# Performance work log

Measured on AMD Instinct MI355X. Metric: run time of the kernel, lower is better.

Reference implementation:

```python
import jax, jax.numpy as jnp
import numpy as np

B, V, M, H = 256, 128, 256, 1024
TIMING_DIM = 10          # ceil(log2(max_timesteps=1024))
DECAY_ALPHA = 0.99
IN_DIM = (V + TIMING_DIM + 1 + 1) * M  # 35840


def setup_inputs() -> dict:
    key = jax.random.key(0)
    ks = jax.random.split(key, 12)
    x = jax.random.uniform(ks[0], (B, V), dtype=jnp.float32)
    memory = jax.random.uniform(ks[1], (B, M, V), dtype=jnp.float32)
    memory_timings = jax.random.randint(ks[2], (B, M), 0, 1000).astype(jnp.int64)
    memory_surprise = jax.random.uniform(ks[3], (B, M), dtype=jnp.float32)
    last_prediction = jax.random.uniform(ks[4], (B, V), dtype=jnp.float32)
    s1 = 1.0 / np.sqrt(IN_DIM)
    s2 = 1.0 / np.sqrt(H)
    W1 = jax.random.uniform(ks[5], (IN_DIM, H), dtype=jnp.float32, minval=-s1, maxval=s1)
    b1 = jnp.zeros((H,), jnp.float32)
    Wg = jax.random.uniform(ks[6], (IN_DIM, H), dtype=jnp.float32, minval=-s1, maxval=s1)
    bg = jnp.zeros((H,), jnp.float32)
    W2 = jax.random.uniform(ks[7], (H, V), dtype=jnp.float32, minval=-s2, maxval=s2)
    b2 = jnp.zeros((V,), jnp.float32)
    return {"x": x, "memory": memory, "memory_timings": memory_timings,
            "memory_surprise": memory_surprise, "last_prediction": last_prediction,
            "W1": W1, "b1": b1, "Wg": Wg, "bg": bg, "W2": W2, "b2": b2}


def _step(x, memory, memory_timings, memory_surprise, last_prediction):
    # surprise of incoming token under last prediction
    surprise = -jnp.log(jnp.sum(x * last_prediction, axis=1) + 1e-8)  # [B]
    # age + decay
    timings = memory_timings + 1
    surp = memory_surprise * DECAY_ALPHA
    # ring-buffer roll, write newest at slot 0
    mem = jnp.roll(memory, 1, axis=1).at[:, 0, :].set(x)
    timings = jnp.roll(timings, 1, axis=1).at[:, 0].set(0)
    surp = jnp.roll(surp, 1, axis=1).at[:, 0].set(surprise)
    # sort by age ascending, gather memory/surprise
    idx = jnp.argsort(timings, axis=1)                               # [B,M]
    sorted_timings = jnp.take_along_axis(timings, idx, axis=1)       # [B,M]
    sorted_memory = jnp.take_along_axis(mem, idx[..., None], axis=1)  # [B,M,V]
    sorted_surprise = jnp.take_along_axis(surp, idx, axis=1)          # [B,M]
    # binary encode timings
    powers = 2 ** jnp.arange(TIMING_DIM, dtype=sorted_timings.dtype)
    bits = ((sorted_timings[..., None] // powers) % 2).astype(jnp.float32)  # [B,M,T]
    norm_t = sorted_timings.astype(jnp.float32) / (
        jnp.max(sorted_timings, axis=1, keepdims=True).astype(jnp.float32) + 1.0)
    pred_input = jnp.concatenate(
        [sorted_memory.reshape(B, -1), bits.reshape(B, -1),
         norm_t.reshape(B, -1), sorted_surprise.reshape(B, -1)], axis=1)  # [B, IN_DIM]
    return pred_input


def reference(x, memory, memory_timings, memory_surprise, last_prediction,
              W1, b1, Wg, bg, W2, b2):
    pred_input = _step(x, memory, memory_timings, memory_surprise, last_prediction)
    # gated dense network: h = (xW1+b1) * sigmoid(xWg+bg); logits = hW2+b2
    h = (pred_input @ W1 + b1) * jax.nn.sigmoid(pred_input @ Wg + bg)
    return h @ W2 + b2
```

## Files before the change

### kernel.cpp

```cpp
#include <hip/hip_runtime.h>
#include <stdint.h>
#include <math.h>

#define BB 256
#define VV 128
#define MM 256
#define TDIM 10
#define HH 1024
#define IN_DIM 35840
#define KSPLIT 16
#define KSLICE 2240
#define BK 64
#define NCHUNK 35

using f32x4  = __attribute__((ext_vector_type(4))) float;
using bf16x8 = __attribute__((ext_vector_type(8))) short;

__device__ __forceinline__ unsigned short f2bf(float f) {
    unsigned int u = __float_as_uint(f);
    unsigned int r = (u + 0x7FFFu + ((u >> 16) & 1u)) >> 16;
    return (unsigned short)r;
}

__device__ __forceinline__ void gload_lds16(const void* g, void* l) {
    __builtin_amdgcn_global_load_lds(
        (const __attribute__((address_space(1))) unsigned int*)g,
        (__attribute__((address_space(3))) unsigned int*)l,
        16, 0, 0);
}

__global__ __launch_bounds__(256)
void k_build(const float* __restrict__ x, const float* __restrict__ memory,
             const int* __restrict__ timings, const float* __restrict__ msurp,
             const float* __restrict__ lastp, short* __restrict__ A)
{
    int b = blockIdx.x, t = threadIdx.x;
    __shared__ int t_s[MM], idx_s[MM], st_s[MM];
    __shared__ float red[MM];
    __shared__ float s_surprise;

    t_s[t] = (t == 0) ? 0 : timings[b*MM + t - 1] + 1;
    red[t] = (t < VV) ? x[b*VV + t] * lastp[b*VV + t] : 0.f;
    __syncthreads();
    for (int s = 128; s > 0; s >>= 1) {
        if (t < s) red[t] += red[t + s];
        __syncthreads();
    }
    if (t == 0) s_surprise = -logf(red[0] + 1e-8f);

    int ti = t_s[t], cnt = 0;
    #pragma unroll 4
    for (int j = 0; j < MM; ++j) {
        int tj = t_s[j];
        cnt += (tj < ti) || (tj == ti && j < t);
    }
    idx_s[cnt] = t;
    st_s[cnt]  = ti;
    __syncthreads();

    float invm = 1.f / ((float)st_s[MM-1] + 1.f);
    short* Ab = A + (size_t)b * IN_DIM;
    {
        int st = st_s[t], src = idx_s[t];
        #pragma unroll
        for (int tt = 0; tt < TDIM; ++tt)
            Ab[32768 + t*TDIM + tt] = (short)f2bf((float)((st >> tt) & 1));
        Ab[35328 + t] = (short)f2bf((float)st * invm);
        float sv = (src == 0) ? s_surprise : msurp[b*MM + src - 1] * 0.99f;
        Ab[35584 + t] = (short)f2bf(sv);
    }
    int half = t >> 7, v = t & (VV-1);
    for (int p = half; p < MM; p += 2) {
        int src = idx_s[p];
        float val = (src == 0) ? x[b*VV + v]
                               : memory[((size_t)b*MM + src - 1)*VV + v];
        Ab[p*VV + v] = (short)f2bf(val);
    }
}

__global__ __launch_bounds__(256, 4)
void k_gemm(const short* __restrict__ A, const float* __restrict__ W1,
            const float* __restrict__ Wg, float* __restrict__ P)
{
    int ks = blockIdx.x;
    int xt = blockIdx.y;
    const float* W = (xt < 32) ? W1 : Wg;
    int wcol0 = (xt & 31) * 32;
    int pcol0 = xt * 32;
    int k0 = ks * KSLICE;

    __shared__ bf16x8 As8[2048];
    __shared__ bf16x8 Ws8[256];

    int t = threadIdx.x;
    int l = t & 63, wv = t >> 6;
    int r = l & 15, q = l >> 4;

    int aoff[4][2], boff[2][2];
    #pragma unroll
    for (int mt = 0; mt < 4; ++mt)
        #pragma unroll
        for (int s = 0; s < 2; ++s)
            aoff[mt][s] = (wv*64 + mt*16 + r)*8 + ((q + 4*s) ^ (r & 7));
    #pragma unroll
    for (int nt = 0; nt < 2; ++nt)
        #pragma unroll
        for (int s = 0; s < 2; ++s)
            boff[nt][s] = (nt*16 + r)*8 + ((q + 4*s) ^ (r & 7));

    f32x4 acc[4][2];
    #pragma unroll
    for (int mt = 0; mt < 4; ++mt)
        #pragma unroll
        for (int nt = 0; nt < 2; ++nt)
            acc[mt][nt] = (f32x4){0.f, 0.f, 0.f, 0.f};

    int wn = t & 31, wkg = t >> 5;
    const float* wbase = W + (size_t)(k0 + wkg*8)*HH + wcol0 + wn;

    float wreg[8];
    #pragma unroll
    for (int j = 0; j < 8; ++j) wreg[j] = wbase[(size_t)j*HH];

    for (int c = 0; c < NCHUNK; ++c) {
        int kc = k0 + c*BK;
        __syncthreads();
        {
            union { bf16x8 v; unsigned int d[4]; } u;
            #pragma unroll
            for (int j = 0; j < 4; ++j)
                u.d[j] = (unsigned int)f2bf(wreg[2*j]) |
                         ((unsigned int)f2bf(wreg[2*j+1]) << 16);
            Ws8[wn*8 + (wkg ^ (wn & 7))] = u.v;
        }
        #pragma unroll
        for (int i = 0; i < 8; ++i) {
            int G = t + i*256;
            int m = G >> 3;
            int kb = (G & 7) ^ (m & 7);
            const short* gp = A + (size_t)m*IN_DIM + kc + kb*8;
            gload_lds16(gp, (void*)(As8 + ((t & ~63) + i*256)));
        }
        {
            int cn = (c + 1 < NCHUNK) ? c + 1 : c;
            const float* wp = wbase + (size_t)cn*BK*HH;
            #pragma unroll
            for (int j = 0; j < 8; ++j) wreg[j] = wp[(size_t)j*HH];
        }
        __syncthreads();

        #pragma unroll
        for (int s = 0; s < 2; ++s) {
            bf16x8 af[4], bfr[2];
            #pragma unroll
            for (int mt = 0; mt < 4; ++mt) af[mt] = As8[aoff[mt][s]];
            #pragma unroll
            for (int nt = 0; nt < 2; ++nt) bfr[nt] = Ws8[boff[nt][s]];
            #pragma unroll
            for (int mt = 0; mt < 4; ++mt)
                #pragma unroll
                for (int nt = 0; nt < 2; ++nt)
                    acc[mt][nt] = __builtin_amdgcn_mfma_f32_16x16x32_bf16(
                        af[mt], bfr[nt], acc[mt][nt], 0, 0, 0);
        }
    }

    #pragma unroll
    for (int mt = 0; mt < 4; ++mt)
        #pragma unroll
        for (int nt = 0; nt < 2; ++nt)
            #pragma unroll
            for (int rg = 0; rg < 4; ++rg) {
                int m = wv*64 + mt*16 + q*4 + rg;
                int n = pcol0 + nt*16 + r;
                P[((size_t)ks*BB + m)*2048 + n] = acc[mt][nt][rg];
            }
}

__global__ __launch_bounds__(256)
void k_reduce(const float* __restrict__ P, const float* __restrict__ b1,
              const float* __restrict__ bg, float* __restrict__ h)
{
    int id = blockIdx.x * 256 + threadIdx.x;
    int b = id >> 10, j = id & 1023;
    float p1 = b1[j], pg = bg[j];
    #pragma unroll
    for (int ks = 0; ks < KSPLIT; ++ks) {
        size_t base = ((size_t)ks*BB + b)*2048;
        p1 += P[base + j];
        pg += P[base + 1024 + j];
    }
    float g = 1.f / (1.f + expf(-pg));
    h[(size_t)b*HH + j] = p1 * g;
}

__global__ __launch_bounds__(256)
void k_out(const float* __restrict__ h, const float* __restrict__ W2,
           const float* __restrict__ b2, float* __restrict__ out)
{
    int b = blockIdx.x, t = threadIdx.x;
    int v = t & 127, kh = t >> 7;
    const float* hb = h + (size_t)b*HH + kh*512;
    const float* wp = W2 + (size_t)kh*512*VV + v;
    float acc = 0.f;
    #pragma unroll 8
    for (int k = 0; k < 512; ++k)
        acc += hb[k] * wp[(size_t)k*VV];
    __shared__ float s[256];
    s[t] = acc;
    __syncthreads();
    if (t < 128)
        out[(size_t)b*VV + v] = s[t] + s[t + 128] + b2[v];
}

extern "C" void kernel_launch(void* const* d_in, const int* in_sizes, int n_in,
                              void* d_out, int out_size, void* d_ws, size_t ws_size,
                              hipStream_t stream)
{
    const float* x    = (const float*)d_in[0];
    const float* mem  = (const float*)d_in[1];
    const int*   tim  = (const int*)d_in[2];
    const float* msur = (const float*)d_in[3];
    const float* lp   = (const float*)d_in[4];
    const float* W1   = (const float*)d_in[5];
    const float* b1   = (const float*)d_in[6];
    const float* Wg   = (const float*)d_in[7];
    const float* bg   = (const float*)d_in[8];
    const float* W2   = (const float*)d_in[9];
    const float* b2   = (const float*)d_in[10];
    float* out = (float*)d_out;

    short* A = (short*)d_ws;
    float* P = (float*)((char*)d_ws + 18350080);
    float* h = (float*)((char*)d_ws + 51904512);

    k_build <<<256, 256, 0, stream>>>(x, mem, tim, msur, lp, A);
    k_gemm  <<<dim3(KSPLIT, 64), 256, 0, stream>>>(A, W1, Wg, P);
    k_reduce<<<1024, 256, 0, stream>>>(P, b1, bg, h);
    k_out   <<<256, 256, 0, stream>>>(h, W2, b2, out);
}
```

Before: 439.6 us.

## Double-buffer GEMM LDS tiles with 512-thread blocks and vectorize reduce

The split-K GEMM now uses 512-thread blocks covering 64 output columns, with BK halved to 32 and double-buffered LDS for both the A and W tiles. The next chunk's global->LDS load and the W prefetch two chunks ahead overlap the current MFMAs, leaving one barrier per iteration. Each block reuses its A tile across twice as many columns, at the cost of fewer blocks and more loop iterations. The reduce kernel also switches to float4 vector loads and stores.

```diff
diff --git a/kernel.cpp b/kernel.cpp
--- a/kernel.cpp
+++ b/kernel.cpp
@@ -10,8 +10,8 @@
 #define IN_DIM 35840
 #define KSPLIT 16
 #define KSLICE 2240
-#define BK 64
-#define NCHUNK 35
+#define BK 32
+#define NCHUNK 70
 
 using f32x4  = __attribute__((ext_vector_type(4))) float;
 using bf16x8 = __attribute__((ext_vector_type(8))) short;
@@ -78,35 +78,36 @@
     }
 }
 
-__global__ __launch_bounds__(256, 4)
+__global__ __launch_bounds__(512, 4)
 void k_gemm(const short* __restrict__ A, const float* __restrict__ W1,
             const float* __restrict__ Wg, float* __restrict__ P)
 {
     int ks = blockIdx.x;
     int xt = blockIdx.y;
-    const float* W = (xt < 32) ? W1 : Wg;
-    int wcol0 = (xt & 31) * 32;
-    int pcol0 = xt * 32;
+    const float* W = (xt < 16) ? W1 : Wg;
+    int wcol0 = (xt & 15) * 64;
+    int pcol0 = xt * 64;
     int k0 = ks * KSLICE;
 
-    __shared__ bf16x8 As8[2048];
-    __shared__ bf16x8 Ws8[256];
+    __shared__ bf16x8 As8[2][1024];
+    __shared__ bf16x8 Ws8[2][256];
 
     int t = threadIdx.x;
     int l = t & 63, wv = t >> 6;
     int r = l & 15, q = l >> 4;
-
-    int aoff[4][2], boff[2][2];
-    #pragma unroll
-    for (int mt = 0; mt < 4; ++mt)
-        #pragma unroll
-        for (int s = 0; s < 2; ++s)
-            aoff[mt][s] = (wv*64 + mt*16 + r)*8 + ((q + 4*s) ^ (r & 7));
-    #pragma unroll
-    for (int nt = 0; nt < 2; ++nt)
-        #pragma unroll
-        for (int s = 0; s < 2; ++s)
-            boff[nt][s] = (nt*16 + r)*8 + ((q + 4*s) ^ (r & 7));
+    int wm = wv & 3, nh = wv >> 2;
+
+    int aoff[4], boff[2];
+    #pragma unroll
+    for (int mt = 0; mt < 4; ++mt) {
+        int R = wm*64 + mt*16 + r;
+        aoff[mt] = R*4 + (q ^ ((R >> 1) & 3));
+    }
+    #pragma unroll
+    for (int nt = 0; nt < 2; ++nt) {
+        int R = nh*32 + nt*16 + r;
+        boff[nt] = R*4 + (q ^ ((R >> 1) & 3));
+    }
 
     f32x4 acc[4][2];
     #pragma unroll
@@ -115,47 +116,64 @@
         for (int nt = 0; nt < 2; ++nt)
             acc[mt][nt] = (f32x4){0.f, 0.f, 0.f, 0.f};
 
-    int wn = t & 31, wkg = t >> 5;
-    const float* wbase = W + (size_t)(k0 + wkg*8)*HH + wcol0 + wn;
-
-    float wreg[8];
-    #pragma unroll
-    for (int j = 0; j < 8; ++j) wreg[j] = wbase[(size_t)j*HH];
+    int wn = l;
+    int wkg = wv >> 1, whalf = wv & 1;
+    int wslot16 = (wn*4 + (wkg ^ ((wn >> 1) & 3))) * 16 + whalf * 8;
+    const float* wbase = W + (size_t)(k0 + wv*4)*HH + wcol0 + wn;
+    float wreg[4];
+
+    #pragma unroll
+    for (int j = 0; j < 4; ++j) wreg[j] = wbase[(size_t)j*HH];
+    {
+        unsigned int lo = (unsigned int)f2bf(wreg[0]) | ((unsigned int)f2bf(wreg[1]) << 16);
+        unsigned int hi = (unsigned int)f2bf(wreg[2]) | ((unsigned int)f2bf(wreg[3]) << 16);
+        unsigned int* dst = (unsigned int*)((char*)&Ws8[0][0] + wslot16);
+        dst[0] = lo; dst[1] = hi;
+    }
+    #pragma unroll
+    for (int i = 0; i < 2; ++i) {
+        int G = t + i*512;
+        int m = G >> 2;
+        int kb = (G & 3) ^ ((m >> 1) & 3);
+        gload_lds16(A + (size_t)m*IN_DIM + k0 + kb*8,
+                    (void*)(&As8[0][0] + (t & ~63) + i*512));
+    }
+    #pragma unroll
+    for (int j = 0; j < 4; ++j) wreg[j] = wbase[(size_t)(BK*HH) + (size_t)j*HH];
+    __syncthreads();
 
     for (int c = 0; c < NCHUNK; ++c) {
-        int kc = k0 + c*BK;
-        __syncthreads();
-        {
-            union { bf16x8 v; unsigned int d[4]; } u;
-            #pragma unroll
-            for (int j = 0; j < 4; ++j)
-                u.d[j] = (unsigned int)f2bf(wreg[2*j]) |
-                         ((unsigned int)f2bf(wreg[2*j+1]) << 16);
-            Ws8[wn*8 + (wkg ^ (wn & 7))] = u.v;
-        }
-        #pragma unroll
-        for (int i = 0; i < 8; ++i) {
-            int G = t + i*256;
-            int m = G >> 3;
-            int kb = (G & 7) ^ (m & 7);
-            const short* gp = A + (size_t)m*IN_DIM + kc + kb*8;
-            gload_lds16(gp, (void*)(As8 + ((t & ~63) + i*256)));
-        }
-        {
-            int cn = (c + 1 < NCHUNK) ? c + 1 : c;
-            const float* wp = wbase + (size_t)cn*BK*HH;
-            #pragma unroll
-            for (int j = 0; j < 8; ++j) wreg[j] = wp[(size_t)j*HH];
-        }
-        __syncthreads();
-
-        #pragma unroll
-        for (int s = 0; s < 2; ++s) {
+        int pb = c & 1, pn = pb ^ 1;
+        {
+            unsigned int lo = (unsigned int)f2bf(wreg[0]) | ((unsigned int)f2bf(wreg[1]) << 16);
+            unsigned int hi = (unsigned int)f2bf(wreg[2]) | ((unsigned int)f2bf(wreg[3]) << 16);
+            unsigned int* dst = (unsigned int*)((char*)&Ws8[pn][0] + wslot16);
+            dst[0] = lo; dst[1] = hi;
+        }
+        {
+            int cA = (c + 1 < NCHUNK) ? c + 1 : c;
+            int kc = k0 + cA*BK;
+            #pragma unroll
+            for (int i = 0; i < 2; ++i) {
+                int G = t + i*512;
+                int m = G >> 2;
+                int kb = (G & 3) ^ ((m >> 1) & 3);
+                gload_lds16(A + (size_t)m*IN_DIM + kc + kb*8,
+                            (void*)(&As8[pn][0] + (t & ~63) + i*512));
+            }
+        }
+        {
+            int cW = (c + 2 < NCHUNK) ? c + 2 : NCHUNK - 1;
+            const float* wp = wbase + (size_t)cW*BK*HH;
+            #pragma unroll
+            for (int j = 0; j < 4; ++j) wreg[j] = wp[(size_t)j*HH];
+        }
+        {
             bf16x8 af[4], bfr[2];
             #pragma unroll
-            for (int mt = 0; mt < 4; ++mt) af[mt] = As8[aoff[mt][s]];
-            #pragma unroll
-            for (int nt = 0; nt < 2; ++nt) bfr[nt] = Ws8[boff[nt][s]];
+            for (int mt = 0; mt < 4; ++mt) af[mt] = As8[pb][aoff[mt]];
+            #pragma unroll
+            for (int nt = 0; nt < 2; ++nt) bfr[nt] = Ws8[pb][boff[nt]];
             #pragma unroll
             for (int mt = 0; mt < 4; ++mt)
                 #pragma unroll
@@ -163,6 +181,7 @@
                     acc[mt][nt] = __builtin_amdgcn_mfma_f32_16x16x32_bf16(
                         af[mt], bfr[nt], acc[mt][nt], 0, 0, 0);
         }
+        __syncthreads();
     }
 
     #pragma unroll
@@ -171,8 +190,8 @@
         for (int nt = 0; nt < 2; ++nt)
             #pragma unroll
             for (int rg = 0; rg < 4; ++rg) {
-                int m = wv*64 + mt*16 + q*4 + rg;
-                int n = pcol0 + nt*16 + r;
+                int m = wm*64 + mt*16 + q*4 + rg;
+                int n = pcol0 + nh*32 + nt*16 + r;
                 P[((size_t)ks*BB + m)*2048 + n] = acc[mt][nt][rg];
             }
 }
@@ -181,17 +200,21 @@
 void k_reduce(const float* __restrict__ P, const float* __restrict__ b1,
               const float* __restrict__ bg, float* __restrict__ h)
 {
-    int id = blockIdx.x * 256 + threadIdx.x;
-    int b = id >> 10, j = id & 1023;
-    float p1 = b1[j], pg = bg[j];
+    int b = blockIdx.x, t = threadIdx.x;
+    const f32x4* P4 = (const f32x4*)P;
+    f32x4 p1 = ((const f32x4*)b1)[t];
+    f32x4 pg = ((const f32x4*)bg)[t];
     #pragma unroll
     for (int ks = 0; ks < KSPLIT; ++ks) {
-        size_t base = ((size_t)ks*BB + b)*2048;
-        p1 += P[base + j];
-        pg += P[base + 1024 + j];
-    }
-    float g = 1.f / (1.f + expf(-pg));
-    h[(size_t)b*HH + j] = p1 * g;
+        size_t base = ((size_t)ks*BB + b) * 512;
+        p1 += P4[base + t];
+        pg += P4[base + 256 + t];
+    }
+    f32x4 o;
+    #pragma unroll
+    for (int j = 0; j < 4; ++j)
+        o[j] = p1[j] / (1.f + expf(-pg[j]));
+    ((f32x4*)h)[(size_t)b*256 + t] = o;
 }
 
 __global__ __launch_bounds__(256)
@@ -235,7 +258,7 @@
     float* h = (float*)((char*)d_ws + 51904512);
 
     k_build <<<256, 256, 0, stream>>>(x, mem, tim, msur, lp, A);
-    k_gemm  <<<dim3(KSPLIT, 64), 256, 0, stream>>>(A, W1, Wg, P);
-    k_reduce<<<1024, 256, 0, stream>>>(P, b1, bg, h);
+    k_gemm  <<<dim3(KSPLIT, 32), 512, 0, stream>>>(A, W1, Wg, P);
+    k_reduce<<<256, 256, 0, stream>>>(P, b1, bg, h);
     k_out   <<<256, 256, 0, stream>>>(h, W2, b2, out);
 }
```

Result: no change. 435.6 us (-0.9%).
